# Kernel tuning notes

Hardware: AMD Instinct MI355X
Metric: run time of the kernel (lower is better)

## Reference

```python
import jax, jax.numpy as jnp
import numpy as np

N, E = 50000, 1600000
H, D = 2, 64            # n_heads, embed_dim (per-head out dim)
L = 3                   # n_layers
EPS = 1e-5


def setup_inputs() -> dict:
    key = jax.random.key(0)
    ks = jax.random.split(key, 16)
    s = 0.1
    return {
        "x": jax.random.normal(ks[0], (N, 64), jnp.float32),
        "src": jax.random.randint(ks[1], (E,), 0, N, jnp.int32),
        "dst": jax.random.randint(ks[2], (E,), 0, N, jnp.int32),
        "emb_w": jax.random.normal(ks[3], (64, 64), jnp.float32) * s,
        "emb_b": jnp.zeros((64,), jnp.float32),
        "fc_w": jax.random.normal(ks[4], (L, H * D, D), jnp.float32) * s,
        "attn_l": jax.random.normal(ks[5], (L, H, D), jnp.float32) * s,
        "attn_r": jax.random.normal(ks[6], (L, H, D), jnp.float32) * s,
        "gat_b": jnp.zeros((L, H * D), jnp.float32),
        "bn1_g": jnp.ones((L, H * D), jnp.float32),
        "bn1_b": jnp.zeros((L, H * D), jnp.float32),
        "ff_w1": jax.random.normal(ks[7], (L, 218, H * D), jnp.float32) * s,
        "ff_b1": jnp.zeros((L, 218), jnp.float32),
        "ff_w2": jax.random.normal(ks[8], (L, D, 218), jnp.float32) * s,
        "ff_b2": jnp.zeros((L, D), jnp.float32),
        "bn2_g": jnp.ones((L, D), jnp.float32),
        "bn2_b": jnp.zeros((L, D), jnp.float32),
        "mlp_w1": jax.random.normal(ks[9], (64, D * (L + 1)), jnp.float32) * s,
        "mlp_bn_g": jnp.ones((64,), jnp.float32),
        "mlp_bn_b": jnp.zeros((64,), jnp.float32),
        "mlp_w2": jax.random.normal(ks[10], (1, 64), jnp.float32) * s,
    }


def batch_norm(h, g, b):
    # BatchNorm1d in training mode: batch mean, biased variance
    mu = h.mean(0)
    var = ((h - mu) ** 2).mean(0)
    return g * (h - mu) * jax.lax.rsqrt(var + EPS) + b


def gat_conv(h, src, dst, fc_w, al, ar, bias):
    n = h.shape[0]
    feat = (h @ fc_w.T).reshape(n, H, D)            # [N,H,D]
    el = (feat * al).sum(-1)                        # [N,H]
    er = (feat * ar).sum(-1)                        # [N,H]
    e = jax.nn.leaky_relu(el[src] + er[dst], 0.2)   # [E,H]
    m = jax.ops.segment_max(e, dst, num_segments=n)
    ex = jnp.exp(e - m[dst])
    den = jax.ops.segment_sum(ex, dst, num_segments=n)
    alpha = ex / den[dst]                           # [E,H]
    out = jax.ops.segment_sum(alpha[:, :, None] * feat[src], dst, num_segments=n)
    return out.reshape(n, H * D) + bias             # flatten(1) + GAT bias


def reference(x, src, dst, emb_w, emb_b, fc_w, attn_l, attn_r, gat_b,
              bn1_g, bn1_b, ff_w1, ff_b1, ff_w2, ff_b2, bn2_g, bn2_b,
              mlp_w1, mlp_bn_g, mlp_bn_b, mlp_w2):
    h = x @ emb_w.T + emb_b
    xs = [h]
    for l in range(L):
        g = gat_conv(h, src, dst, fc_w[l], attn_l[l], attn_r[l], gat_b[l])
        g = batch_norm(g, bn1_g[l], bn1_b[l])
        g = jax.nn.relu(g @ ff_w1[l].T + ff_b1[l]) @ ff_w2[l].T + ff_b2[l]
        h = batch_norm(g, bn2_g[l], bn2_b[l])
        xs.append(h)
    h = jnp.concatenate(xs, axis=1)                 # JumpingKnowledge('cat')
    h = jax.nn.relu(batch_norm(h @ mlp_w1.T, mlp_bn_g, mlp_bn_b))
    return h @ mlp_w2.T                             # [N, out_dim]
```

## Files before the change

### kernel.cpp

```cpp
#include <hip/hip_runtime.h>
#include <cstdint>

#define BN_EPS 1e-5f

typedef _Float16 f16x8 __attribute__((ext_vector_type(8)));
typedef _Float16 f16x2 __attribute__((ext_vector_type(2)));
typedef float f32x4 __attribute__((ext_vector_type(4)));

__device__ __forceinline__ unsigned short f2h(float f) {
  _Float16 h = (_Float16)f;
  return *(unsigned short*)&h;
}
__device__ __forceinline__ float2 h2f2(unsigned int q) {
  f16x2 h = __builtin_bit_cast(f16x2, q);
  return make_float2((float)h.x, (float)h.y);
}

#define CHUNK 8192
#define MAXBUK 512

__global__ __launch_bounds__(256) void k_bcount(const int* __restrict__ dst, int* __restrict__ bcnt, int E) {
  __shared__ int hist[MAXBUK];
  int tid = threadIdx.x;
  int base = blockIdx.x * CHUNK;
  int cnt = min(CHUNK, E - base);
  if (cnt <= 0) return;
  for (int b = tid; b < MAXBUK; b += 256) hist[b] = 0;
  __syncthreads();
  for (int i = tid; i < cnt; i += 256) atomicAdd(&hist[dst[base + i] >> 7], 1);
  __syncthreads();
  for (int b = tid; b < MAXBUK; b += 256) {
    int c = hist[b];
    if (c > 0) atomicAdd(&bcnt[b], c);
  }
}

__global__ __launch_bounds__(512) void k_bscan(const int* __restrict__ bcnt, int* __restrict__ bcur,
                                               int* __restrict__ bbase, int nbuk) {
  __shared__ int sh[512];
  int t = threadIdx.x;
  int v = (t < nbuk) ? bcnt[t] : 0;
  sh[t] = v;
  __syncthreads();
  for (int off = 1; off < 512; off <<= 1) {
    int u = (t >= off) ? sh[t - off] : 0;
    __syncthreads();
    sh[t] += u;
    __syncthreads();
  }
  if (t < nbuk) {
    int excl = sh[t] - v;
    bcur[t] = excl;
    bbase[t] = excl;
  }
}

__global__ __launch_bounds__(256) void k_bucket(const int* __restrict__ src, const int* __restrict__ dst,
                                                int* __restrict__ bcur, unsigned int* __restrict__ pairs,
                                                int E) {
  __shared__ unsigned int ep[CHUNK];
  __shared__ int bcnt[MAXBUK];
  __shared__ int gbase[MAXBUK];
  __shared__ int rcnt[MAXBUK];
  int tid = threadIdx.x;
  int base = blockIdx.x * CHUNK;
  int cnt = min(CHUNK, E - base);
  if (cnt <= 0) return;

  for (int b = tid; b < MAXBUK; b += 256) { bcnt[b] = 0; rcnt[b] = 0; }
  __syncthreads();
  for (int i = tid; i < cnt; i += 256) {
    int d = dst[base + i];
    int s = src[base + i];
    unsigned int pk = ((unsigned)(d >> 7) << 23) | ((unsigned)(d & 127) << 16) | (unsigned)s;
    ep[i] = pk;
    atomicAdd(&bcnt[d >> 7], 1);
  }
  __syncthreads();
  for (int b = tid; b < MAXBUK; b += 256) {
    int c = bcnt[b];
    gbase[b] = (c > 0) ? atomicAdd(&bcur[b], c) : 0;
  }
  __syncthreads();
  for (int i = tid; i < cnt; i += 256) {
    unsigned int pk = ep[i];
    int bk = pk >> 23;
    int r = atomicAdd(&rcnt[bk], 1);
    pairs[gbase[bk] + r] = pk & 0x007FFFFFu;
  }
}

#define PLACE_CAP 24576

__global__ __launch_bounds__(256) void k_place(const int* __restrict__ bbase,
                                               const unsigned int* __restrict__ pairs,
                                               unsigned short* __restrict__ csr16,
                                               int* __restrict__ rowptr, int n, int nbuk, int E) {
  __shared__ unsigned short stage[PLACE_CAP];
  __shared__ int nc[128];
  __shared__ int nstart[128];
  __shared__ int nrun[128];
  int tid = threadIdx.x;
  int bk = blockIdx.x;
  int v0 = bk * 128;
  int beg = bbase[bk];
  int end = (bk + 1 < nbuk) ? bbase[bk + 1] : E;
  int cnt = end - beg;
  if (tid < 128) { nc[tid] = 0; nrun[tid] = 0; }
  __syncthreads();
  for (int i = tid; i < cnt; i += 256) atomicAdd(&nc[(pairs[beg + i] >> 16) & 127], 1);
  __syncthreads();
  if (tid < 128) nstart[tid] = nc[tid];
  __syncthreads();
  for (int off = 1; off < 128; off <<= 1) {
    int v = (tid < 128 && tid >= off) ? nstart[tid - off] : 0;
    __syncthreads();
    if (tid < 128) nstart[tid] += v;
    __syncthreads();
  }
  if (tid < 128) nstart[tid] -= nc[tid];
  __syncthreads();
  if (tid < 128 && v0 + tid < n) rowptr[v0 + tid] = beg + nstart[tid];
  if (bk == nbuk - 1 && tid == 0) rowptr[n] = E;
  if (cnt <= 0) return;
  if (cnt <= PLACE_CAP) {
    for (int i = tid; i < cnt; i += 256) {
      unsigned int p = pairs[beg + i];
      int dlow = (p >> 16) & 127;
      int r = atomicAdd(&nrun[dlow], 1);
      stage[nstart[dlow] + r] = (unsigned short)(p & 0xFFFF);
    }
    __syncthreads();
    for (int i = tid; i < cnt; i += 256) csr16[beg + i] = stage[i];
  } else {
    for (int i = tid; i < cnt; i += 256) {
      unsigned int p = pairs[beg + i];
      int dlow = (p >> 16) & 127;
      int r = atomicAdd(&nrun[dlow], 1);
      csr16[beg + nstart[dlow] + r] = (unsigned short)(p & 0xFFFF);
    }
  }
}

__global__ __launch_bounds__(256) void k_cvtw(
    const float* __restrict__ emb, const float* __restrict__ fc,
    const float* __restrict__ w2, const float* __restrict__ mlp,
    unsigned short* __restrict__ o_emb, unsigned short* __restrict__ o_fc,
    unsigned short* __restrict__ o_w2, unsigned short* __restrict__ o_mlp,
    int n_emb, int n_fc, int n_w2rows, int n_mlp) {
  int idx = blockIdx.x * 256 + threadIdx.x;
  if (idx < n_emb) { o_emb[idx] = f2h(emb[idx]); return; }
  idx -= n_emb;
  if (idx < n_fc) { o_fc[idx] = f2h(fc[idx]); return; }
  idx -= n_fc;
  int w2tot = n_w2rows * 224;
  if (idx < w2tot) {
    int r = idx / 224, c = idx - r * 224;
    o_w2[idx] = f2h((c < 218) ? w2[r * 218 + c] : 0.f);
    return;
  }
  idx -= w2tot;
  if (idx < n_mlp) o_mlp[idx] = f2h(mlp[idx]);
}

__global__ __launch_bounds__(256) void k_foldw1(const float* __restrict__ W1, const float* __restrict__ b1,
                                                const float* __restrict__ stats, const float* __restrict__ gam,
                                                const float* __restrict__ bet, float invM,
                                                unsigned short* __restrict__ W16, float* __restrict__ b1p,
                                                int rows, int K) {
  __shared__ float aA[128];
  __shared__ float aB[128];
  int tid = threadIdx.x;
  if (tid < K) {
    float mean = stats[tid] * invM;
    float var = stats[K + tid] * invM - mean * mean;
    float a = gam[tid] * rsqrtf(var + BN_EPS);
    aA[tid] = a;
    aB[tid] = bet[tid] - mean * a;
  }
  __syncthreads();
  int w = tid >> 6, lane = tid & 63;
  int i = blockIdx.x * 4 + w;
  if (i >= rows) return;
  const float* wr = W1 + (size_t)i * K;
  float dot = 0.f;
  for (int k = lane; k < K; k += 64) {
    float wv = wr[k];
    W16[(size_t)i * K + k] = f2h(wv * aA[k]);
    dot += wv * aB[k];
  }
  for (int o = 32; o > 0; o >>= 1) dot += __shfl_down(dot, o, 64);
  if (lane == 0) b1p[i] = b1[i] + dot;
}

__global__ __launch_bounds__(256) void k_gemm(
    const void* __restrict__ Xv, int xpitch,
    const void* __restrict__ Wv, int wpitch,
    const float* __restrict__ bias,
    const float* __restrict__ stats, const float* __restrict__ gamma, const float* __restrict__ beta,
    float invM, void* __restrict__ Yv, int ypitch,
    int M, int KK, int COLS, int flags,
    float* __restrict__ ostats,
    const float* __restrict__ al, const float* __restrict__ ar,
    float* __restrict__ el, float* __restrict__ er) {
  __shared__ unsigned short Xs[128 * 72];
  __shared__ unsigned short Ws[64 * 72];
  __shared__ float affA[256];
  __shared__ float affB[256];

  int tid = threadIdx.x;
  int m0 = blockIdx.x * 128;
  int c0 = blockIdx.y * 64;
  const bool relu = (flags & 1) != 0;
  const bool aff = (flags & 2) != 0;
  const bool yf16 = (flags & 4) != 0;
  const bool xf16 = (flags & 8) != 0;
  const bool fstat = (flags & 16) != 0;
  const bool fattn = (flags & 32) != 0;
  const bool wf16 = (flags & 64) != 0;

  if (aff) {
    if (tid < KK && tid < 256) {
      float mean = stats[tid] * invM;
      float var = stats[KK + tid] * invM - mean * mean;
      float a = gamma[tid] * rsqrtf(var + BN_EPS);
      affA[tid] = a;
      affB[tid] = beta[tid] - mean * a;
    }
    __syncthreads();
  }

  int w = tid >> 6;
  int lane = tid & 63;
  int l15 = lane & 15;
  int lhi = lane >> 4;

  f32x4 acc[2][4];
#pragma unroll
  for (int i = 0; i < 2; ++i)
#pragma unroll
    for (int j = 0; j < 4; ++j) acc[i][j] = (f32x4){0.f, 0.f, 0.f, 0.f};

  for (int kt = 0; kt < KK; kt += 64) {
    if (xf16) {
      const unsigned short* X16 = (const unsigned short*)Xv;
#pragma unroll
      for (int p = 0; p < 4; ++p) {
        int idx = p * 256 + tid;
        int r = idx >> 3;
        int k8 = (idx & 7) * 8;
        int gr = m0 + r, gk = kt + k8;
        if (gr < M && gk + 8 <= KK) {
          *(uint4*)&Xs[r * 72 + k8] = *(const uint4*)(X16 + (size_t)gr * xpitch + gk);
        } else {
#pragma unroll
          for (int j = 0; j < 8; ++j)
            Xs[r * 72 + k8 + j] =
                (gr < M && gk + j < KK) ? X16[(size_t)gr * xpitch + gk + j] : (unsigned short)0;
        }
      }
    } else {
      const float* X = (const float*)Xv;
      int rb = tid >> 4;
      int c4 = (tid & 15) * 4;
#pragma unroll
      for (int p = 0; p < 8; ++p) {
        int r = p * 16 + rb;
        int gr = m0 + r;
        int gk = kt + c4;
        float4 v = make_float4(0.f, 0.f, 0.f, 0.f);
        if (gr < M) {
          const float* px = X + (size_t)gr * xpitch;
          if (gk + 3 < KK) {
            v = *(const float4*)(px + gk);
            if (aff) {
              v.x = v.x * affA[gk] + affB[gk];
              v.y = v.y * affA[gk + 1] + affB[gk + 1];
              v.z = v.z * affA[gk + 2] + affB[gk + 2];
              v.w = v.w * affA[gk + 3] + affB[gk + 3];
            }
          } else if (gk < KK) {
            float tmp[4];
#pragma unroll
            for (int j = 0; j < 4; ++j) {
              float t = 0.f;
              if (gk + j < KK) {
                t = px[gk + j];
                if (aff) t = t * affA[gk + j] + affB[gk + j];
              }
              tmp[j] = t;
            }
            v.x = tmp[0]; v.y = tmp[1]; v.z = tmp[2]; v.w = tmp[3];
          }
        }
        ushort4 o = make_ushort4(f2h(v.x), f2h(v.y), f2h(v.z), f2h(v.w));
        *(ushort4*)&Xs[r * 72 + c4] = o;
      }
    }
    if (wf16) {
      const unsigned short* W16 = (const unsigned short*)Wv;
#pragma unroll
      for (int p = 0; p < 4; ++p) {
        int idx = p * 256 + tid;
        int c = idx >> 4;
        int k4 = (idx & 15) * 4;
        int gc = c0 + c, gk = kt + k4;
        uint2 val = make_uint2(0u, 0u);
        if (gc < COLS && gk + 4 <= wpitch) {
          val = *(const uint2*)(W16 + (size_t)gc * wpitch + gk);
        }
        *(uint2*)&Ws[c * 72 + k4] = val;
      }
    } else {
      const float* W = (const float*)Wv;
      int cb = tid >> 5;
      int k2 = (tid & 31) * 2;
#pragma unroll
      for (int p = 0; p < 8; ++p) {
        int c = p * 8 + cb;
        int gc = c0 + c;
        int gk = kt + k2;
        float2 v = make_float2(0.f, 0.f);
        if (gc < COLS) {
          const float* pw = W + (size_t)gc * wpitch;
          if (gk + 1 < KK) {
            v = *(const float2*)(pw + gk);
          } else if (gk < KK) {
            v.x = pw[gk];
          }
        }
        ushort2 o = make_ushort2(f2h(v.x), f2h(v.y));
        *(ushort2*)&Ws[c * 72 + k2] = o;
      }
    }
    __syncthreads();

#pragma unroll
    for (int ks = 0; ks < 64; ks += 32) {
      f16x8 a0 = *(const f16x8*)&Xs[(32 * w + l15) * 72 + ks + lhi * 8];
      f16x8 a1 = *(const f16x8*)&Xs[(32 * w + 16 + l15) * 72 + ks + lhi * 8];
#pragma unroll
      for (int ct = 0; ct < 4; ++ct) {
        f16x8 b = *(const f16x8*)&Ws[(16 * ct + l15) * 72 + ks + lhi * 8];
        acc[0][ct] = __builtin_amdgcn_mfma_f32_16x16x32_f16(a0, b, acc[0][ct], 0, 0, 0);
        acc[1][ct] = __builtin_amdgcn_mfma_f32_16x16x32_f16(a1, b, acc[1][ct], 0, 0, 0);
      }
    }
    __syncthreads();
  }

  float sArr[4] = {0.f, 0.f, 0.f, 0.f}, qArr[4] = {0.f, 0.f, 0.f, 0.f};
  float rdl[8], rdr[8];
#pragma unroll
  for (int j = 0; j < 8; ++j) { rdl[j] = 0.f; rdr[j] = 0.f; }

#pragma unroll
  for (int rt = 0; rt < 2; ++rt) {
#pragma unroll
    for (int ct = 0; ct < 4; ++ct) {
      int c = c0 + 16 * ct + l15;
      if (c >= COLS) continue;
      float bv = bias ? bias[c] : 0.f;
      float alc = fattn ? al[c] : 0.f;
      float arc = fattn ? ar[c] : 0.f;
#pragma unroll
      for (int reg = 0; reg < 4; ++reg) {
        int r = m0 + 32 * w + 16 * rt + lhi * 4 + reg;
        if (r >= M) continue;
        float vv = acc[rt][ct][reg] + bv;
        if (relu) vv = fmaxf(vv, 0.f);
        if (yf16)
          ((unsigned short*)Yv)[(size_t)r * ypitch + c] = f2h(vv);
        else
          ((float*)Yv)[(size_t)r * ypitch + c] = vv;
        if (fstat) { sArr[ct] += vv; qArr[ct] += vv * vv; }
        if (fattn) { rdl[rt * 4 + reg] += vv * alc; rdr[rt * 4 + reg] += vv * arc; }
      }
    }
  }

  if (fattn) {
#pragma unroll
    for (int j = 0; j < 8; ++j) {
      float a = rdl[j], b = rdr[j];
      a += __shfl_xor(a, 1, 64); b += __shfl_xor(b, 1, 64);
      a += __shfl_xor(a, 2, 64); b += __shfl_xor(b, 2, 64);
      a += __shfl_xor(a, 4, 64); b += __shfl_xor(b, 4, 64);
      a += __shfl_xor(a, 8, 64); b += __shfl_xor(b, 8, 64);
      rdl[j] = a; rdr[j] = b;
    }
    if (l15 == 0) {
      int hy = blockIdx.y;
#pragma unroll
      for (int j = 0; j < 8; ++j) {
        int r = m0 + 32 * w + 16 * (j >> 2) + lhi * 4 + (j & 3);
        if (r < M) {
          el[(size_t)r * 2 + hy] = rdl[j];
          er[(size_t)r * 2 + hy] = rdr[j];
        }
      }
    }
  }

  if (fstat) {
#pragma unroll
    for (int ct = 0; ct < 4; ++ct) {
      float s = sArr[ct], q = qArr[ct];
      s += __shfl_xor(s, 16, 64); q += __shfl_xor(q, 16, 64);
      s += __shfl_xor(s, 32, 64); q += __shfl_xor(q, 32, 64);
      if (lhi == 0) {
        affA[w * 64 + ct * 16 + l15] = s;
        affB[w * 64 + ct * 16 + l15] = q;
      }
    }
    __syncthreads();
    if (tid < 64) {
      float s = affA[tid] + affA[64 + tid] + affA[128 + tid] + affA[192 + tid];
      float q = affB[tid] + affB[64 + tid] + affB[128 + tid] + affB[192 + tid];
      atomicAdd(&ostats[tid], s);
      atomicAdd(&ostats[64 + tid], q);
    }
  }
}

__global__ __launch_bounds__(256) void k_agg(const int* __restrict__ rowptr,
                                             const unsigned short* __restrict__ csr16,
                                             const unsigned short* __restrict__ feat16,
                                             const float* __restrict__ el,
                                             const float* __restrict__ er, const float* __restrict__ gatb,
                                             unsigned short* __restrict__ g16, int n) {
  int v = blockIdx.x * 4 + (threadIdx.x >> 6);
  if (v >= n) return;
  int lane = threadIdx.x & 63;
  int grp = lane >> 5;
  int sub = lane & 31;
  int head = sub >> 4;
  int beg = rowptr[v], end = rowptr[v + 1];
  float er0 = er[(size_t)v * 2 + 0], er1 = er[(size_t)v * 2 + 1];
  float s0 = 0.f, s1 = 0.f;
  float a0 = 0.f, a1 = 0.f, a2 = 0.f, a3 = 0.f;
  const char* fb = (const char*)feat16;
  int sub8 = sub * 8;
  for (int base = beg; base < end; base += 64) {
    int nch = min(64, end - base);
    int uoff_l = 0;
    float w0_l = 0.f, w1_l = 0.f;
    if (base + lane < end) {
      int u = csr16[base + lane];
      uoff_l = u * 256;
      float2 tt = *(const float2*)&el[(size_t)u * 2];
      float e0 = tt.x + er0, e1 = tt.y + er1;
      e0 = (e0 > 0.f) ? e0 : 0.2f * e0;
      e1 = (e1 > 0.f) ? e1 : 0.2f * e1;
      w0_l = __expf(e0);
      w1_l = __expf(e1);
      s0 += w0_l;
      s1 += w1_l;
    }
    int i = 0;
    for (; i + 16 <= nch; i += 16) {
      uint2 q[8];
#pragma unroll
      for (int p = 0; p < 8; ++p) {
        int e = i + 2 * p + grp;
        int uo = __shfl(uoff_l, e);
        q[p] = *(const uint2*)(fb + (size_t)(unsigned)uo + sub8);
      }
#pragma unroll
      for (int p = 0; p < 8; ++p) {
        int e = i + 2 * p + grp;
        float wa = __shfl(w0_l, e);
        float wb = __shfl(w1_l, e);
        float wgt = head ? wb : wa;
        float2 fx = h2f2(q[p].x);
        float2 fy = h2f2(q[p].y);
        a0 += wgt * fx.x;
        a1 += wgt * fx.y;
        a2 += wgt * fy.x;
        a3 += wgt * fy.y;
      }
    }
    for (; i + 8 <= nch; i += 8) {
      uint2 q[4];
#pragma unroll
      for (int p = 0; p < 4; ++p) {
        int e = i + 2 * p + grp;
        int uo = __shfl(uoff_l, e);
        q[p] = *(const uint2*)(fb + (size_t)(unsigned)uo + sub8);
      }
#pragma unroll
      for (int p = 0; p < 4; ++p) {
        int e = i + 2 * p + grp;
        float wa = __shfl(w0_l, e);
        float wb = __shfl(w1_l, e);
        float wgt = head ? wb : wa;
        float2 fx = h2f2(q[p].x);
        float2 fy = h2f2(q[p].y);
        a0 += wgt * fx.x;
        a1 += wgt * fx.y;
        a2 += wgt * fy.x;
        a3 += wgt * fy.y;
      }
    }
    for (; i < nch; i += 2) {
      int e = i + grp;
      int ec = min(e, nch - 1);
      int uo = __shfl(uoff_l, ec);
      float wa = __shfl(w0_l, ec);
      float wb = __shfl(w1_l, ec);
      float wgt = head ? wb : wa;
      if (e >= nch) wgt = 0.f;
      uint2 q = *(const uint2*)(fb + (size_t)(unsigned)uo + sub8);
      float2 fx = h2f2(q.x);
      float2 fy = h2f2(q.y);
      a0 += wgt * fx.x;
      a1 += wgt * fx.y;
      a2 += wgt * fy.x;
      a3 += wgt * fy.y;
    }
  }
  a0 += __shfl_xor(a0, 32, 64);
  a1 += __shfl_xor(a1, 32, 64);
  a2 += __shfl_xor(a2, 32, 64);
  a3 += __shfl_xor(a3, 32, 64);
  for (int o = 32; o > 0; o >>= 1) {
    s0 += __shfl_xor(s0, o, 64);
    s1 += __shfl_xor(s1, o, 64);
  }
  if (lane < 32) {
    float s = head ? s1 : s0;
    float inv = (end > beg) ? 1.f / s : 0.f;
    int c = 4 * sub;
    ushort4 o4;
    o4.x = f2h(a0 * inv + gatb[c]);
    o4.y = f2h(a1 * inv + gatb[c + 1]);
    o4.z = f2h(a2 * inv + gatb[c + 2]);
    o4.w = f2h(a3 * inv + gatb[c + 3]);
    *(ushort4*)&g16[(size_t)v * 128 + c] = o4;
  }
}

__global__ __launch_bounds__(256) void k_colstats16(const unsigned short* __restrict__ Z, int pitch,
                                                    int C, int M, float* __restrict__ stats) {
  __shared__ float ls[256];
  __shared__ float lq[256];
  int t = threadIdx.x;
  int c = t % C;
  int rpb = 256 / C;
  int r = blockIdx.x * rpb + t / C;
  int stride = gridDim.x * rpb;
  float s = 0.f, q = 0.f;
  const _Float16* Zh = (const _Float16*)Z;
  for (; r < M; r += stride) {
    float v = (float)Zh[(size_t)r * pitch + c];
    s += v;
    q += v * v;
  }
  ls[t] = s;
  lq[t] = q;
  __syncthreads();
  if (t < C) {
    for (int i = 1; i < rpb; ++i) {
      s += ls[t + i * C];
      q += lq[t + i * C];
    }
    atomicAdd(&stats[c], s);
    atomicAdd(&stats[C + c], q);
  }
}

__global__ __launch_bounds__(256) void k_bnapply(const float* __restrict__ u, const float* __restrict__ stats,
                                                 const float* __restrict__ gam, const float* __restrict__ bet,
                                                 unsigned short* __restrict__ yout, int n, float invM) {
  int idx = blockIdx.x * 256 + threadIdx.x;
  if (idx >= n * 16) return;
  int r = idx >> 4, c4 = (idx & 15) * 4;
  float4 uu = *(const float4*)&u[(size_t)r * 64 + c4];
  float vv[4] = {uu.x, uu.y, uu.z, uu.w};
  ushort4 o;
  unsigned short* op = (unsigned short*)&o;
#pragma unroll
  for (int j = 0; j < 4; ++j) {
    int c = c4 + j;
    float mean = stats[c] * invM;
    float var = stats[64 + c] * invM - mean * mean;
    float a = gam[c] * rsqrtf(var + BN_EPS);
    float b = bet[c] - mean * a;
    op[j] = f2h(a * vv[j] + b);
  }
  *(ushort4*)&yout[(size_t)r * 256 + c4] = o;
}

__global__ __launch_bounds__(256) void k_final(const float* __restrict__ y, const float* __restrict__ stats,
                                               const float* __restrict__ gam, const float* __restrict__ bet,
                                               const float* __restrict__ w2, float* __restrict__ out, int n,
                                               float invM) {
  int v = blockIdx.x * 4 + (threadIdx.x >> 6);
  if (v >= n) return;
  int lane = threadIdx.x & 63;
  float mean = stats[lane] * invM;
  float var = stats[64 + lane] * invM - mean * mean;
  float a = gam[lane] * rsqrtf(var + BN_EPS);
  float b = bet[lane] - mean * a;
  float h = a * y[(size_t)v * 64 + lane] + b;
  h = fmaxf(h, 0.f) * w2[lane];
  for (int o = 32; o > 0; o >>= 1) h += __shfl_down(h, o, 64);
  if (lane == 0) out[v] = h;
}

extern "C" void kernel_launch(void* const* d_in, const int* in_sizes, int n_in,
                              void* d_out, int out_size, void* d_ws, size_t ws_size,
                              hipStream_t stream) {
  const float* x = (const float*)d_in[0];
  const int* src = (const int*)d_in[1];
  const int* dst = (const int*)d_in[2];
  const float* emb_w = (const float*)d_in[3];
  const float* emb_b = (const float*)d_in[4];
  const float* fc_w = (const float*)d_in[5];
  const float* attn_l = (const float*)d_in[6];
  const float* attn_r = (const float*)d_in[7];
  const float* gat_b = (const float*)d_in[8];
  const float* bn1_g = (const float*)d_in[9];
  const float* bn1_b = (const float*)d_in[10];
  const float* ff_w1 = (const float*)d_in[11];
  const float* ff_b1 = (const float*)d_in[12];
  const float* ff_w2 = (const float*)d_in[13];
  const float* ff_b2 = (const float*)d_in[14];
  const float* bn2_g = (const float*)d_in[15];
  const float* bn2_b = (const float*)d_in[16];
  const float* mlp_w1 = (const float*)d_in[17];
  const float* mlp_bn_g = (const float*)d_in[18];
  const float* mlp_bn_b = (const float*)d_in[19];
  const float* mlp_w2 = (const float*)d_in[20];
  float* out = (float*)d_out;
  (void)n_in;
  (void)out_size;

  const int n = in_sizes[0] / 64;
  const int E = in_sizes[1];
  const int NL = 3;
  const int nbuk = (n + 127) >> 7;

  char* wsb = (char*)d_ws;
  size_t off = 0;
  auto alloc = [&](size_t bytes) {
    size_t o = off;
    off = (off + bytes + 255) & ~(size_t)255;
    return o;
  };
  size_t o_bcnt = alloc((size_t)512 * 4);
  size_t o_stats = alloc(1280 * 4);
  size_t zero_bytes = off;
  size_t o_rowptr = alloc((size_t)(n + 1) * 4);
  size_t o_bcur = alloc((size_t)512 * 4);
  size_t o_bbase = alloc((size_t)512 * 4);
  size_t o_csr = alloc((size_t)E * 2);
  size_t o_pairs = alloc((size_t)E * 4);
  size_t o_feat = alloc((size_t)n * 64 * 4);
  size_t o_g = alloc((size_t)n * 128 * 2);
  size_t o_t = alloc((size_t)n * 224 * 2 + 256);
  size_t o_xs = alloc((size_t)n * 256 * 2);
  size_t o_el = alloc((size_t)n * 2 * 4);
  size_t o_er = alloc((size_t)n * 2 * 4);
  const int n_emb = 64 * 64;
  const int n_fc = NL * 128 * 64;
  const int n_w2rows = NL * 64;
  const int n_mlp = 64 * 256;
  size_t o_embw = alloc((size_t)n_emb * 2);
  size_t o_fcw = alloc((size_t)n_fc * 2);
  size_t o_w2w = alloc((size_t)n_w2rows * 224 * 2);
  size_t o_mlpw = alloc((size_t)n_mlp * 2);
  size_t o_w1f = alloc((size_t)218 * 128 * 2);
  size_t o_b1p = alloc((size_t)224 * 4);
  if (off > ws_size) return;

  int* bcnt = (int*)(wsb + o_bcnt);
  float* stats = (float*)(wsb + o_stats);
  int* rowptr = (int*)(wsb + o_rowptr);
  int* bcur = (int*)(wsb + o_bcur);
  int* bbase = (int*)(wsb + o_bbase);
  unsigned short* csr16 = (unsigned short*)(wsb + o_csr);
  unsigned int* pairs = (unsigned int*)(wsb + o_pairs);
  unsigned short* feat16 = (unsigned short*)(wsb + o_feat);
  unsigned short* g16 = (unsigned short*)(wsb + o_g);
  unsigned short* t16 = (unsigned short*)(wsb + o_t);
  unsigned short* xs16 = (unsigned short*)(wsb + o_xs);
  float* el = (float*)(wsb + o_el);
  float* er = (float*)(wsb + o_er);
  unsigned short* embw16 = (unsigned short*)(wsb + o_embw);
  unsigned short* fcw16 = (unsigned short*)(wsb + o_fcw);
  unsigned short* w2w16 = (unsigned short*)(wsb + o_w2w);
  unsigned short* mlpw16 = (unsigned short*)(wsb + o_mlpw);
  unsigned short* w1f16 = (unsigned short*)(wsb + o_w1f);
  float* b1p = (float*)(wsb + o_b1p);
  float* u = (float*)(wsb + o_feat);

  hipMemsetAsync(d_ws, 0, zero_bytes, stream);

  int gchunk = (E + CHUNK - 1) / CHUNK;
  k_bcount<<<gchunk, 256, 0, stream>>>(dst, bcnt, E);
  k_bscan<<<1, 512, 0, stream>>>(bcnt, bcur, bbase, nbuk);
  k_bucket<<<gchunk, 256, 0, stream>>>(src, dst, bcur, pairs, E);
  k_place<<<nbuk, 256, 0, stream>>>(bbase, pairs, csr16, rowptr, n, nbuk, E);

  int cvt_total = n_emb + n_fc + n_w2rows * 224 + n_mlp;
  k_cvtw<<<(cvt_total + 255) / 256, 256, 0, stream>>>(emb_w, fc_w, ff_w2, mlp_w1,
                                                      embw16, fcw16, w2w16, mlpw16,
                                                      n_emb, n_fc, n_w2rows, n_mlp);

  int gm = (n + 127) / 128;
  float invM = 1.f / (float)n;

  k_gemm<<<dim3(gm, 1), 256, 0, stream>>>(x, 64, embw16, 64, emb_b, nullptr, nullptr, nullptr, invM,
                                          xs16, 256, n, 64, 64, 4 | 64,
                                          nullptr, nullptr, nullptr, nullptr, nullptr);

  for (int l = 0; l < NL; ++l) {
    float* sbn1 = stats + l * 384;
    float* sbn2 = stats + l * 384 + 256;
    k_gemm<<<dim3(gm, 2), 256, 0, stream>>>(xs16 + 64 * l, 256, fcw16 + (size_t)l * 128 * 64, 64,
                                            nullptr, nullptr, nullptr, nullptr, invM,
                                            feat16, 128, n, 64, 128, 4 | 8 | 32 | 64,
                                            nullptr, attn_l + l * 128, attn_r + l * 128, el, er);
    k_agg<<<(n + 3) / 4, 256, 0, stream>>>(rowptr, csr16, feat16, el, er, gat_b + l * 128, g16, n);
    k_colstats16<<<512, 256, 0, stream>>>(g16, 128, 128, n, sbn1);
    k_foldw1<<<(218 + 3) / 4, 256, 0, stream>>>(ff_w1 + (size_t)l * 218 * 128, ff_b1 + l * 218,
                                                sbn1, bn1_g + l * 128, bn1_b + l * 128, invM,
                                                w1f16, b1p, 218, 128);
    k_gemm<<<dim3(gm, 4), 256, 0, stream>>>(g16, 128, w1f16, 128, b1p,
                                            nullptr, nullptr, nullptr, invM,
                                            t16, 224, n, 128, 218, 1 | 4 | 8 | 64,
                                            nullptr, nullptr, nullptr, nullptr, nullptr);
    k_gemm<<<dim3(gm, 1), 256, 0, stream>>>(t16, 224, w2w16 + (size_t)l * 64 * 224, 224, ff_b2 + l * 64,
                                            nullptr, nullptr, nullptr, invM,
                                            u, 64, n, 218, 64, 8 | 16 | 64,
                                            sbn2, nullptr, nullptr, nullptr, nullptr);
    k_bnapply<<<(n * 16 + 255) / 256, 256, 0, stream>>>(u, sbn2, bn2_g + l * 64, bn2_b + l * 64,
                                                        xs16 + 64 * (l + 1), n, invM);
  }

  float* smlp = stats + 1152;
  k_gemm<<<dim3(gm, 1), 256, 0, stream>>>(xs16, 256, mlpw16, 256, nullptr, nullptr, nullptr, nullptr, invM,
                                          u, 64, n, 256, 64, 8 | 16 | 64,
                                          smlp, nullptr, nullptr, nullptr, nullptr);
  k_final<<<(n + 3) / 4, 256, 0, stream>>>(u, smlp, mlp_bn_g, mlp_bn_b, mlp_w2, out, n, invM);
}
```

Measured before the change: 665.0 us.

## Template GEMM column tile; fuse BN2 apply into next layer fc GEMM

The GEMM kernel gets a template parameter for the number of 16-column tiles. The fc GEMM now covers both heads in one block (NCT=8), so the X tile is loaded once and el/er for both heads come out together. For layers after the first, the BN2 normalisation is applied inside the fc GEMM's X load from the fp32 u buffer, and the normalised fp16 rows are written to the xs jumping-knowledge buffer. That removes the separate bnapply launch except on the last layer. The FF1 GEMM also uses wider 128-column tiles, which raises LDS and register use per block and may lower occupancy.

```diff
diff --git a/kernel.cpp b/kernel.cpp
--- a/kernel.cpp
+++ b/kernel.cpp
@@ -193,6 +193,7 @@
   if (lane == 0) b1p[i] = b1[i] + dot;
 }
 
+template <int NCT>
 __global__ __launch_bounds__(256) void k_gemm(
     const void* __restrict__ Xv, int xpitch,
     const void* __restrict__ Wv, int wpitch,
@@ -202,15 +203,16 @@
     int M, int KK, int COLS, int flags,
     float* __restrict__ ostats,
     const float* __restrict__ al, const float* __restrict__ ar,
-    float* __restrict__ el, float* __restrict__ er) {
+    float* __restrict__ el, float* __restrict__ er,
+    unsigned short* __restrict__ xsout) {
   __shared__ unsigned short Xs[128 * 72];
-  __shared__ unsigned short Ws[64 * 72];
+  __shared__ unsigned short Ws[NCT * 16 * 72];
   __shared__ float affA[256];
   __shared__ float affB[256];
 
   int tid = threadIdx.x;
   int m0 = blockIdx.x * 128;
-  int c0 = blockIdx.y * 64;
+  int c0 = blockIdx.y * (NCT * 16);
   const bool relu = (flags & 1) != 0;
   const bool aff = (flags & 2) != 0;
   const bool yf16 = (flags & 4) != 0;
@@ -235,11 +237,11 @@
   int l15 = lane & 15;
   int lhi = lane >> 4;
 
-  f32x4 acc[2][4];
+  f32x4 acc[2][NCT];
 #pragma unroll
   for (int i = 0; i < 2; ++i)
 #pragma unroll
-    for (int j = 0; j < 4; ++j) acc[i][j] = (f32x4){0.f, 0.f, 0.f, 0.f};
+    for (int j = 0; j < NCT; ++j) acc[i][j] = (f32x4){0.f, 0.f, 0.f, 0.f};
 
   for (int kt = 0; kt < KK; kt += 64) {
     if (xf16) {
@@ -295,12 +297,13 @@
         }
         ushort4 o = make_ushort4(f2h(v.x), f2h(v.y), f2h(v.z), f2h(v.w));
         *(ushort4*)&Xs[r * 72 + c4] = o;
+        if (xsout && gr < M) *(ushort4*)&xsout[(size_t)gr * 256 + c4] = o;
       }
     }
     if (wf16) {
       const unsigned short* W16 = (const unsigned short*)Wv;
 #pragma unroll
-      for (int p = 0; p < 4; ++p) {
+      for (int p = 0; p < NCT; ++p) {
         int idx = p * 256 + tid;
         int c = idx >> 4;
         int k4 = (idx & 15) * 4;
@@ -340,7 +343,7 @@
       f16x8 a0 = *(const f16x8*)&Xs[(32 * w + l15) * 72 + ks + lhi * 8];
       f16x8 a1 = *(const f16x8*)&Xs[(32 * w + 16 + l15) * 72 + ks + lhi * 8];
 #pragma unroll
-      for (int ct = 0; ct < 4; ++ct) {
+      for (int ct = 0; ct < NCT; ++ct) {
         f16x8 b = *(const f16x8*)&Ws[(16 * ct + l15) * 72 + ks + lhi * 8];
         acc[0][ct] = __builtin_amdgcn_mfma_f32_16x16x32_f16(a0, b, acc[0][ct], 0, 0, 0);
         acc[1][ct] = __builtin_amdgcn_mfma_f32_16x16x32_f16(a1, b, acc[1][ct], 0, 0, 0);
@@ -349,15 +352,19 @@
     __syncthreads();
   }
 
-  float sArr[4] = {0.f, 0.f, 0.f, 0.f}, qArr[4] = {0.f, 0.f, 0.f, 0.f};
-  float rdl[8], rdr[8];
-#pragma unroll
-  for (int j = 0; j < 8; ++j) { rdl[j] = 0.f; rdr[j] = 0.f; }
+  float sArr[NCT], qArr[NCT];
+#pragma unroll
+  for (int j = 0; j < NCT; ++j) { sArr[j] = 0.f; qArr[j] = 0.f; }
+  float rdl[2][8], rdr[2][8];
+#pragma unroll
+  for (int h = 0; h < 2; ++h)
+#pragma unroll
+    for (int j = 0; j < 8; ++j) { rdl[h][j] = 0.f; rdr[h][j] = 0.f; }
 
 #pragma unroll
   for (int rt = 0; rt < 2; ++rt) {
 #pragma unroll
-    for (int ct = 0; ct < 4; ++ct) {
+    for (int ct = 0; ct < NCT; ++ct) {
       int c = c0 + 16 * ct + l15;
       if (c >= COLS) continue;
       float bv = bias ? bias[c] : 0.f;
@@ -374,29 +381,36 @@
         else
           ((float*)Yv)[(size_t)r * ypitch + c] = vv;
         if (fstat) { sArr[ct] += vv; qArr[ct] += vv * vv; }
-        if (fattn) { rdl[rt * 4 + reg] += vv * alc; rdr[rt * 4 + reg] += vv * arc; }
+        if (fattn) {
+          int h = ct >> 2;
+          rdl[h][rt * 4 + reg] += vv * alc;
+          rdr[h][rt * 4 + reg] += vv * arc;
+        }
       }
     }
   }
 
   if (fattn) {
 #pragma unroll
-    for (int j = 0; j < 8; ++j) {
-      float a = rdl[j], b = rdr[j];
-      a += __shfl_xor(a, 1, 64); b += __shfl_xor(b, 1, 64);
-      a += __shfl_xor(a, 2, 64); b += __shfl_xor(b, 2, 64);
-      a += __shfl_xor(a, 4, 64); b += __shfl_xor(b, 4, 64);
-      a += __shfl_xor(a, 8, 64); b += __shfl_xor(b, 8, 64);
-      rdl[j] = a; rdr[j] = b;
-    }
+    for (int h = 0; h < 2; ++h)
+#pragma unroll
+      for (int j = 0; j < 8; ++j) {
+        float a = rdl[h][j], b = rdr[h][j];
+        a += __shfl_xor(a, 1, 64); b += __shfl_xor(b, 1, 64);
+        a += __shfl_xor(a, 2, 64); b += __shfl_xor(b, 2, 64);
+        a += __shfl_xor(a, 4, 64); b += __shfl_xor(b, 4, 64);
+        a += __shfl_xor(a, 8, 64); b += __shfl_xor(b, 8, 64);
+        rdl[h][j] = a; rdr[h][j] = b;
+      }
     if (l15 == 0) {
-      int hy = blockIdx.y;
 #pragma unroll
       for (int j = 0; j < 8; ++j) {
         int r = m0 + 32 * w + 16 * (j >> 2) + lhi * 4 + (j & 3);
         if (r < M) {
-          el[(size_t)r * 2 + hy] = rdl[j];
-          er[(size_t)r * 2 + hy] = rdr[j];
+          el[(size_t)r * 2 + 0] = rdl[0][j];
+          el[(size_t)r * 2 + 1] = rdl[1][j];
+          er[(size_t)r * 2 + 0] = rdr[0][j];
+          er[(size_t)r * 2 + 1] = rdr[1][j];
         }
       }
     }
@@ -404,7 +418,7 @@
 
   if (fstat) {
 #pragma unroll
-    for (int ct = 0; ct < 4; ++ct) {
+    for (int ct = 0; ct < NCT; ++ct) {
       float s = sArr[ct], q = qArr[ct];
       s += __shfl_xor(s, 16, 64); q += __shfl_xor(q, 16, 64);
       s += __shfl_xor(s, 32, 64); q += __shfl_xor(q, 32, 64);
@@ -656,7 +670,8 @@
   size_t o_bbase = alloc((size_t)512 * 4);
   size_t o_csr = alloc((size_t)E * 2);
   size_t o_pairs = alloc((size_t)E * 4);
-  size_t o_feat = alloc((size_t)n * 64 * 4);
+  size_t o_feat = alloc((size_t)n * 128 * 2);
+  size_t o_u = alloc((size_t)n * 64 * 4);
   size_t o_g = alloc((size_t)n * 128 * 2);
   size_t o_t = alloc((size_t)n * 224 * 2 + 256);
   size_t o_xs = alloc((size_t)n * 256 * 2);
@@ -682,6 +697,7 @@
   unsigned short* csr16 = (unsigned short*)(wsb + o_csr);
   unsigned int* pairs = (unsigned int*)(wsb + o_pairs);
   unsigned short* feat16 = (unsigned short*)(wsb + o_feat);
+  float* u = (float*)(wsb + o_u);
   unsigned short* g16 = (unsigned short*)(wsb + o_g);
   unsigned short* t16 = (unsigned short*)(wsb + o_t);
   unsigned short* xs16 = (unsigned short*)(wsb + o_xs);
@@ -693,7 +709,6 @@
   unsigned short* mlpw16 = (unsigned short*)(wsb + o_mlpw);
   unsigned short* w1f16 = (unsigned short*)(wsb + o_w1f);
   float* b1p = (float*)(wsb + o_b1p);
-  float* u = (float*)(wsb + o_feat);
 
   hipMemsetAsync(d_ws, 0, zero_bytes, stream);
 
@@ -711,37 +726,48 @@
   int gm = (n + 127) / 128;
   float invM = 1.f / (float)n;
 
-  k_gemm<<<dim3(gm, 1), 256, 0, stream>>>(x, 64, embw16, 64, emb_b, nullptr, nullptr, nullptr, invM,
-                                          xs16, 256, n, 64, 64, 4 | 64,
-                                          nullptr, nullptr, nullptr, nullptr, nullptr);
+  k_gemm<4><<<dim3(gm, 1), 256, 0, stream>>>(x, 64, embw16, 64, emb_b, nullptr, nullptr, nullptr, invM,
+                                             xs16, 256, n, 64, 64, 4 | 64,
+                                             nullptr, nullptr, nullptr, nullptr, nullptr, nullptr);
 
   for (int l = 0; l < NL; ++l) {
     float* sbn1 = stats + l * 384;
     float* sbn2 = stats + l * 384 + 256;
-    k_gemm<<<dim3(gm, 2), 256, 0, stream>>>(xs16 + 64 * l, 256, fcw16 + (size_t)l * 128 * 64, 64,
-                                            nullptr, nullptr, nullptr, nullptr, invM,
-                                            feat16, 128, n, 64, 128, 4 | 8 | 32 | 64,
-                                            nullptr, attn_l + l * 128, attn_r + l * 128, el, er);
+    if (l == 0) {
+      k_gemm<8><<<dim3(gm, 1), 256, 0, stream>>>(xs16, 256, fcw16, 64,
+                                                 nullptr, nullptr, nullptr, nullptr, invM,
+                                                 feat16, 128, n, 64, 128, 4 | 8 | 32 | 64,
+                                                 nullptr, attn_l, attn_r, el, er, nullptr);
+    } else {
+      float* sprev = stats + (l - 1) * 384 + 256;
+      k_gemm<8><<<dim3(gm, 1), 256, 0, stream>>>(u, 64, fcw16 + (size_t)l * 128 * 64, 64,
+                                                 nullptr, sprev, bn2_g + (l - 1) * 64, bn2_b + (l - 1) * 64,
+                                                 invM, feat16, 128, n, 64, 128, 2 | 4 | 32 | 64,
+                                                 nullptr, attn_l + l * 128, attn_r + l * 128, el, er,
+                                                 xs16 + 64 * l);
+    }
     k_agg<<<(n + 3) / 4, 256, 0, stream>>>(rowptr, csr16, feat16, el, er, gat_b + l * 128, g16, n);
     k_colstats16<<<512, 256, 0, stream>>>(g16, 128, 128, n, sbn1);
     k_foldw1<<<(218 + 3) / 4, 256, 0, stream>>>(ff_w1 + (size_t)l * 218 * 128, ff_b1 + l * 218,
                                                 sbn1, bn1_g + l * 128, bn1_b + l * 128, invM,
                                                 w1f16, b1p, 218, 128);
-    k_gemm<<<dim3(gm, 4), 256, 0, stream>>>(g16, 128, w1f16, 128, b1p,
-                                            nullptr, nullptr, nullptr, invM,
-                                            t16, 224, n, 128, 218, 1 | 4 | 8 | 64,
-                                            nullptr, nullptr, nullptr, nullptr, nullptr);
-    k_gemm<<<dim3(gm, 1), 256, 0, stream>>>(t16, 224, w2w16 + (size_t)l * 64 * 224, 224, ff_b2 + l * 64,
-                                            nullptr, nullptr, nullptr, invM,
-                                            u, 64, n, 218, 64, 8 | 16 | 64,
-                                            sbn2, nullptr, nullptr, nullptr, nullptr);
-    k_bnapply<<<(n * 16 + 255) / 256, 256, 0, stream>>>(u, sbn2, bn2_g + l * 64, bn2_b + l * 64,
-                                                        xs16 + 64 * (l + 1), n, invM);
+    k_gemm<8><<<dim3(gm, 2), 256, 0, stream>>>(g16, 128, w1f16, 128, b1p,
+                                               nullptr, nullptr, nullptr, invM,
+                                               t16, 224, n, 128, 218, 1 | 4 | 8 | 64,
+                                               nullptr, nullptr, nullptr, nullptr, nullptr, nullptr);
+    k_gemm<4><<<dim3(gm, 1), 256, 0, stream>>>(t16, 224, w2w16 + (size_t)l * 64 * 224, 224, ff_b2 + l * 64,
+                                               nullptr, nullptr, nullptr, invM,
+                                               u, 64, n, 218, 64, 8 | 16 | 64,
+                                               sbn2, nullptr, nullptr, nullptr, nullptr, nullptr);
+    if (l == NL - 1) {
+      k_bnapply<<<(n * 16 + 255) / 256, 256, 0, stream>>>(u, sbn2, bn2_g + l * 64, bn2_b + l * 64,
+                                                          xs16 + 64 * (l + 1), n, invM);
+    }
   }
 
   float* smlp = stats + 1152;
-  k_gemm<<<dim3(gm, 1), 256, 0, stream>>>(xs16, 256, mlpw16, 256, nullptr, nullptr, nullptr, nullptr, invM,
-                                          u, 64, n, 256, 64, 8 | 16 | 64,
-                                          smlp, nullptr, nullptr, nullptr, nullptr);
+  k_gemm<4><<<dim3(gm, 1), 256, 0, stream>>>(xs16, 256, mlpw16, 256, nullptr, nullptr, nullptr, nullptr,
+                                             invM, u, 64, n, 256, 64, 8 | 16 | 64,
+                                             smlp, nullptr, nullptr, nullptr, nullptr, nullptr);
   k_final<<<(n + 3) / 4, 256, 0, stream>>>(u, smlp, mlp_bn_g, mlp_bn_b, mlp_w2, out, n, invM);
 }
```

New measurement: 716.0 us. 7.7% more time.
